# Optimization experiments

Measured on AMD Instinct MI355X. Metric: run time of the kernel, lower is better.

The kernel has to match this reference:

```python
import jax, jax.numpy as jnp
import numpy as np

HIDDEN = 2048
N_HEADS = 16
N_KV = 4
HEAD_DIM = 128
THETA = 500000.0
FREQ_ALLOC = 20  # t section; h = w = (HEAD_DIM//2 - 20)//2 = 22
T = 2048


def setup_inputs() -> dict:
    key = jax.random.key(0)
    k1, k2, k3, k4 = jax.random.split(key, 4)
    positions = jax.random.randint(k1, (3, T), 0, 1024, dtype=jnp.int32)
    hidden_states = jax.random.normal(k2, (T, HIDDEN), dtype=jnp.float32)
    w_qkv = jax.random.normal(k3, (HIDDEN, (N_HEADS + 2 * N_KV) * HEAD_DIM), dtype=jnp.float32) * 0.02
    w_o = jax.random.normal(k4, (N_HEADS * HEAD_DIM, HIDDEN), dtype=jnp.float32) * 0.02
    return {"positions": positions, "hidden_states": hidden_states, "w_qkv": w_qkv, "w_o": w_o}


def _mrope_cos_sin(positions):
    # standard rope table evaluated at positions: cos/sin each [3, T, HEAD_DIM//2]
    inv_freq = 1.0 / (THETA ** (jnp.arange(0, HEAD_DIM, 2, dtype=jnp.float32) / HEAD_DIM))
    freqs = positions.astype(jnp.float32)[..., None] * inv_freq
    cos, sin = jnp.cos(freqs), jnp.sin(freqs)
    sh = (HEAD_DIM // 2 - FREQ_ALLOC) // 2  # 22

    def section(c):
        c_t = c[0, :, -FREQ_ALLOC:]          # time dims from t-positions
        c_h = c[1, :, 0:2 * sh:2]            # even low-freq dims from h-positions
        c_w = c[2, :, 1:2 * sh:2]            # odd low-freq dims from w-positions
        c_hw = jnp.stack([c_h, c_w], axis=-1).reshape(c_h.shape[0], 2 * sh)
        return jnp.concatenate([c_hw, c_t], axis=-1)  # [T, HEAD_DIM//2]

    return section(cos), section(sin)


def _rotate_interleaved(x, cos, sin):
    # is_neox_style=False: even/odd interleaved rotation. x: [T, H, HEAD_DIM]
    x1, x2 = x[..., 0::2], x[..., 1::2]
    c, s = cos[:, None, :], sin[:, None, :]
    o1 = x1 * c - x2 * s
    o2 = x2 * c + x1 * s
    return jnp.stack([o1, o2], axis=-1).reshape(x.shape)


def reference(positions, hidden_states, w_qkv, w_o):
    q_size = N_HEADS * HEAD_DIM
    kv_size = N_KV * HEAD_DIM
    qkv = hidden_states @ w_qkv  # [T, 3072]
    q = qkv[:, :q_size].reshape(T, N_HEADS, HEAD_DIM)
    k = qkv[:, q_size:q_size + kv_size].reshape(T, N_KV, HEAD_DIM)
    v = qkv[:, q_size + kv_size:].reshape(T, N_KV, HEAD_DIM)

    cos, sin = _mrope_cos_sin(positions)
    q = _rotate_interleaved(q, cos, sin)
    k = _rotate_interleaved(k, cos, sin)

    # GQA causal attention
    rep = N_HEADS // N_KV
    kr = jnp.repeat(k, rep, axis=1)  # [T, N_HEADS, D]
    vr = jnp.repeat(v, rep, axis=1)
    scale = HEAD_DIM ** -0.5
    scores = jnp.einsum('qhd,khd->hqk', q, kr) * scale
    causal = jnp.tril(jnp.ones((T, T), dtype=bool))
    scores = jnp.where(causal[None], scores, jnp.finfo(scores.dtype).min)
    attn = jax.nn.softmax(scores, axis=-1)
    out = jnp.einsum('hqk,khd->qhd', attn, vr).reshape(T, N_HEADS * HEAD_DIM)
    return out @ w_o
```

## Files before the change

kernel.cpp:

```cpp
#include <hip/hip_runtime.h>
#include <math.h>

#define T 2048
#define HIDDEN 2048
#define NH 16
#define NKV 4
#define HD 128
#define QKV_N 3072
#define Q_SIZE 2048
#define KV_SIZE 512

typedef __attribute__((ext_vector_type(8))) short short8;
typedef __attribute__((ext_vector_type(4))) short short4v;
typedef __attribute__((ext_vector_type(4))) float floatx4;

__device__ __forceinline__ unsigned short f2bf(float f) {
    union { float f; unsigned int u; } v; v.f = f;
    unsigned int u = v.u;
    u += 0x7fffu + ((u >> 16) & 1u);
    return (unsigned short)(u >> 16);
}

__device__ __forceinline__ void gload_lds16(const unsigned short* g, unsigned short* l) {
    __builtin_amdgcn_global_load_lds((const __attribute__((address_space(1))) unsigned int*)g,
                                     (__attribute__((address_space(3))) unsigned int*)l, 16, 0, 0);
}

__global__ __launch_bounds__(256) void prep_misc(const float* __restrict__ hidden,
                                                 const float* __restrict__ w_qkv,
                                                 const float* __restrict__ w_o,
                                                 const int* __restrict__ positions,
                                                 unsigned short* __restrict__ hb,
                                                 unsigned short* __restrict__ wqt,
                                                 unsigned short* __restrict__ wot,
                                                 float* __restrict__ cosT,
                                                 float* __restrict__ sinT) {
    __shared__ float tile[32][33];
    const int b = blockIdx.x;
    const int tid = threadIdx.x;
    const int tx = tid & 31, ty = tid >> 5;

    if (b < 4096) {
        int i = (b * 256 + tid) * 4;
        float4 v = *(const float4*)(hidden + i);
        hb[i]     = f2bf(v.x);
        hb[i + 1] = f2bf(v.y);
        hb[i + 2] = f2bf(v.z);
        hb[i + 3] = f2bf(v.w);
    } else if (b < 10240) {
        int idx = b - 4096;
        int c0 = (idx % 96) * 32, r0 = (idx / 96) * 32;
#pragma unroll
        for (int i = 0; i < 4; ++i)
            tile[ty + i * 8][tx] = w_qkv[(long)(r0 + ty + i * 8) * QKV_N + c0 + tx];
        __syncthreads();
#pragma unroll
        for (int i = 0; i < 4; ++i)
            wqt[(long)(c0 + ty + i * 8) * HIDDEN + r0 + tx] = f2bf(tile[tx][ty + i * 8]);
    } else if (b < 14336) {
        int idx = b - 10240;
        int c0 = (idx % 64) * 32, r0 = (idx / 64) * 32;
#pragma unroll
        for (int i = 0; i < 4; ++i)
            tile[ty + i * 8][tx] = w_o[(long)(r0 + ty + i * 8) * HIDDEN + c0 + tx];
        __syncthreads();
#pragma unroll
        for (int i = 0; i < 4; ++i)
            wot[(long)(c0 + ty + i * 8) * HIDDEN + r0 + tx] = f2bf(tile[tx][ty + i * 8]);
    } else {
        int idx = b - 14336;
        int t = idx * 4 + (tid >> 6);
        int j = tid & 63;
        int row = (j >= 44) ? 0 : ((j & 1) ? 2 : 1);
        int pos = positions[row * T + t];
        float invf = exp2f((float)j * -0.29580571f);
        float ang = (float)pos * invf;
        cosT[t * 64 + j] = cosf(ang);
        sinT[t * 64 + j] = sinf(ang);
    }
}

__global__ __launch_bounds__(256) void gemm_qkv(const unsigned short* __restrict__ A,
                                                const unsigned short* __restrict__ B,
                                                const float* __restrict__ cosT,
                                                const float* __restrict__ sinT,
                                                unsigned short* __restrict__ qb,
                                                unsigned short* __restrict__ kb,
                                                unsigned short* __restrict__ vt) {
    __shared__ __align__(16) unsigned short As[2][64 * 32];
    __shared__ __align__(16) unsigned short Bs[2][128 * 32];
    const int K = HIDDEN;
    const int tid = threadIdx.x;
    const int wv = tid >> 6;
    const int lane = tid & 63;
    const int m = lane & 15, qd = lane >> 4;
    const unsigned short* Ab = A + (long)(blockIdx.x * 64) * K;
    const unsigned short* Bb = B + (long)(blockIdx.y * 128) * K;
    const int srow = tid >> 2;
    const int scol = (tid & 3) * 8;

    floatx4 acc[4][2];
#pragma unroll
    for (int i = 0; i < 4; ++i)
#pragma unroll
        for (int j = 0; j < 2; ++j) acc[i][j] = (floatx4){0.f, 0.f, 0.f, 0.f};

#define QKV_STAGE(buf, k0)                                                                \
    do {                                                                                  \
        gload_lds16(Ab + (long)srow * K + (k0) + scol,        &As[buf][wv * 512]);        \
        gload_lds16(Bb + (long)srow * K + (k0) + scol,        &Bs[buf][wv * 512]);        \
        gload_lds16(Bb + (long)(64 + srow) * K + (k0) + scol, &Bs[buf][2048 + wv * 512]); \
    } while (0)

    QKV_STAGE(0, 0);
    int cur = 0;
    for (int k0 = 0; k0 < K; k0 += 32) {
        __syncthreads();
        if (k0 + 32 < K) QKV_STAGE(cur ^ 1, k0 + 32);
        short8 a[4], b[2];
#pragma unroll
        for (int i = 0; i < 4; ++i) a[i] = *(const short8*)&As[cur][(i * 16 + m) * 32 + qd * 8];
#pragma unroll
        for (int j = 0; j < 2; ++j) b[j] = *(const short8*)&Bs[cur][(wv * 32 + j * 16 + m) * 32 + qd * 8];
#pragma unroll
        for (int i = 0; i < 4; ++i)
#pragma unroll
            for (int j = 0; j < 2; ++j)
                acc[i][j] = __builtin_amdgcn_mfma_f32_16x16x32_bf16(a[i], b[j], acc[i][j], 0, 0, 0);
        cur ^= 1;
    }
#undef QKV_STAGE

    const int by = blockIdx.y;
    if (by < 20) {
        const float sgn = (m & 1) ? 1.f : -1.f;
        const float qscale = 0.08838834764831845f;
#pragma unroll
        for (int i = 0; i < 4; ++i) {
#pragma unroll
            for (int r = 0; r < 4; ++r) {
                const int t = blockIdx.x * 64 + i * 16 + qd * 4 + r;
                const float* ct = cosT + t * 64;
                const float* st = sinT + t * 64;
#pragma unroll
                for (int j = 0; j < 2; ++j) {
                    const int cq = wv * 32 + j * 16 + m;
                    const int j2 = cq >> 1;
                    float val = acc[i][j][r];
                    float prt = __shfl_xor(val, 1);
                    float o = val * ct[j2] + sgn * prt * st[j2];
                    const int col = by * 128 + cq;
                    if (by < 16) qb[(long)t * Q_SIZE + col] = f2bf(o * qscale);
                    else         kb[(long)t * KV_SIZE + (col - 2048)] = f2bf(o);
                }
            }
        }
    } else {
        const int g = by - 20;
#pragma unroll
        for (int i = 0; i < 4; ++i)
#pragma unroll
            for (int j = 0; j < 2; ++j) {
                const int d = wv * 32 + j * 16 + m;
                const int t0 = blockIdx.x * 64 + i * 16 + qd * 4;
                unsigned short o4[4];
#pragma unroll
                for (int r = 0; r < 4; ++r) o4[r] = f2bf(acc[i][j][r]);
                *(short4v*)&vt[((long)g * HD + d) * T + t0] = *(short4v*)o4;
            }
    }
}

__global__ __launch_bounds__(256) void gemm_out(const unsigned short* __restrict__ A,
                                                const unsigned short* __restrict__ B,
                                                float* __restrict__ C,
                                                int K, int ldc) {
    __shared__ __align__(16) unsigned short As[2][64 * 32];
    __shared__ __align__(16) unsigned short Bs[2][128 * 32];
    const int tid = threadIdx.x;
    const int wv = tid >> 6;
    const int lane = tid & 63;
    const int m = lane & 15, qd = lane >> 4;
    const unsigned short* Ab = A + (long)(blockIdx.x * 64) * K;
    const unsigned short* Bb = B + (long)(blockIdx.y * 128) * K;
    const int srow = tid >> 2;
    const int scol = (tid & 3) * 8;

    floatx4 acc[4][2];
#pragma unroll
    for (int i = 0; i < 4; ++i)
#pragma unroll
        for (int j = 0; j < 2; ++j) acc[i][j] = (floatx4){0.f, 0.f, 0.f, 0.f};

#define OUT_STAGE(buf, k0)                                                                \
    do {                                                                                  \
        gload_lds16(Ab + (long)srow * K + (k0) + scol,        &As[buf][wv * 512]);        \
        gload_lds16(Bb + (long)srow * K + (k0) + scol,        &Bs[buf][wv * 512]);        \
        gload_lds16(Bb + (long)(64 + srow) * K + (k0) + scol, &Bs[buf][2048 + wv * 512]); \
    } while (0)

    OUT_STAGE(0, 0);
    int cur = 0;
    for (int k0 = 0; k0 < K; k0 += 32) {
        __syncthreads();
        if (k0 + 32 < K) OUT_STAGE(cur ^ 1, k0 + 32);
        short8 a[4], b[2];
#pragma unroll
        for (int i = 0; i < 4; ++i) a[i] = *(const short8*)&As[cur][(i * 16 + m) * 32 + qd * 8];
#pragma unroll
        for (int j = 0; j < 2; ++j) b[j] = *(const short8*)&Bs[cur][(wv * 32 + j * 16 + m) * 32 + qd * 8];
#pragma unroll
        for (int i = 0; i < 4; ++i)
#pragma unroll
            for (int j = 0; j < 2; ++j)
                acc[i][j] = __builtin_amdgcn_mfma_f32_16x16x32_bf16(a[i], b[j], acc[i][j], 0, 0, 0);
        cur ^= 1;
    }
#undef OUT_STAGE

#pragma unroll
    for (int i = 0; i < 4; ++i)
#pragma unroll
        for (int j = 0; j < 2; ++j)
#pragma unroll
            for (int r = 0; r < 4; ++r)
                C[(long)(blockIdx.x * 64 + i * 16 + qd * 4 + r) * ldc +
                  blockIdx.y * 128 + wv * 32 + j * 16 + m] = acc[i][j][r];
}

__global__ __launch_bounds__(256, 2) void flash_attn(const unsigned short* __restrict__ qb,
                                                     const unsigned short* __restrict__ kb,
                                                     const unsigned short* __restrict__ vt,
                                                     float* __restrict__ Opart,
                                                     float* __restrict__ MLpart) {
    __shared__ __align__(16) unsigned short Kbuf[2][64 * 128];
    __shared__ __align__(16) unsigned short Vbuf[128 * 64];
    __shared__ __align__(16) unsigned short Pls[4][32 * 72];

    const int tid = threadIdx.x;
    const int wv = tid >> 6;
    const int lane = tid & 63;
    const int m = lane & 15;
    const int qd = lane >> 4;

    const int h = blockIdx.x >> 4;
    const int c16 = blockIdx.x & 15;
    const int g = h >> 2;
    unsigned short* myP = Pls[wv];

    for (int seg = 0; seg < 2; ++seg) {
        const int qt = seg ? (15 - c16) : c16;
        const int half = seg;
        const int n0 = qt + 1;
        const int jt0 = half ? n0 : 0;
        const int jt1 = half ? 2 * qt + 2 : n0;
        const int q0 = qt * 128;

        short8 aq[2][4];
#pragma unroll
        for (int s = 0; s < 2; ++s)
#pragma unroll
            for (int kk = 0; kk < 4; ++kk)
                aq[s][kk] = *(const short8*)(qb + (long)(q0 + s * 64 + wv * 16 + m) * Q_SIZE +
                                             h * HD + kk * 32 + qd * 8);

        floatx4 acc_o[2][8];
#pragma unroll
        for (int s = 0; s < 2; ++s)
#pragma unroll
            for (int nb = 0; nb < 8; ++nb) acc_o[s][nb] = (floatx4){0.f, 0.f, 0.f, 0.f};
        float mrow[2] = {-1e30f, -1e30f};
        float lrow[2] = {0.f, 0.f};

#pragma unroll
        for (int i = 0; i < 4; ++i) {
            int s_ = i * 256 + tid;
            int r = s_ >> 4, c = (s_ & 15) ^ (r & 15);
            gload_lds16(kb + (long)(jt0 * 64 + r) * KV_SIZE + g * HD + c * 8,
                        &Kbuf[0][i * 2048 + wv * 512]);
        }
        int cur = 0;
        for (int jt = jt0; jt < jt1; ++jt) {
            __syncthreads();

            if (jt + 1 < jt1) {
#pragma unroll
                for (int i = 0; i < 4; ++i) {
                    int s_ = i * 256 + tid;
                    int r = s_ >> 4, c = (s_ & 15) ^ (r & 15);
                    gload_lds16(kb + (long)((jt + 1) * 64 + r) * KV_SIZE + g * HD + c * 8,
                                &Kbuf[cur ^ 1][i * 2048 + wv * 512]);
                }
            }
#pragma unroll
            for (int i = 0; i < 4; ++i) {
                int s_ = i * 256 + tid;
                int r = s_ >> 3, c = (s_ & 7) ^ (r & 7);
                gload_lds16(vt + ((long)g * HD + r) * T + jt * 64 + c * 8,
                            &Vbuf[i * 2048 + wv * 512]);
            }

            floatx4 acc_s[2][4];
#pragma unroll
            for (int s = 0; s < 2; ++s)
#pragma unroll
                for (int c = 0; c < 4; ++c) acc_s[s][c] = (floatx4){0.f, 0.f, 0.f, 0.f};
#pragma unroll
            for (int kk = 0; kk < 4; ++kk) {
#pragma unroll
                for (int c = 0; c < 4; ++c) {
                    short8 ak = *(const short8*)&Kbuf[cur][(c * 16 + m) * 128 +
                                                           (((4 * kk + qd) ^ m) * 8)];
                    acc_s[0][c] = __builtin_amdgcn_mfma_f32_16x16x32_bf16(ak, aq[0][kk], acc_s[0][c], 0, 0, 0);
                    acc_s[1][c] = __builtin_amdgcn_mfma_f32_16x16x32_bf16(ak, aq[1][kk], acc_s[1][c], 0, 0, 0);
                }
            }

#pragma unroll
            for (int s = 0; s < 2; ++s) {
                const int dg = 2 * qt + s;
                if (jt >= dg) {
                    const bool full = (jt > dg);
#pragma unroll
                    for (int c = 0; c < 4; ++c)
#pragma unroll
                        for (int r = 0; r < 4; ++r)
                            if (full || (c * 16 + qd * 4 + r > wv * 16 + m)) acc_s[s][c][r] = -1e30f;
                }
                float mx = acc_s[s][0][0];
#pragma unroll
                for (int c = 0; c < 4; ++c)
#pragma unroll
                    for (int r = 0; r < 4; ++r) mx = fmaxf(mx, acc_s[s][c][r]);
                mx = fmaxf(mx, __shfl_xor(mx, 16));
                mx = fmaxf(mx, __shfl_xor(mx, 32));
                float mnew = fmaxf(mrow[s], mx);
                float alpha = __expf(mrow[s] - mnew);
                mrow[s] = mnew;

                float pv[4][4];
                float lsum = 0.f;
#pragma unroll
                for (int c = 0; c < 4; ++c)
#pragma unroll
                    for (int r = 0; r < 4; ++r) {
                        pv[c][r] = __expf(acc_s[s][c][r] - mnew);
                        lsum += pv[c][r];
                    }
                lsum += __shfl_xor(lsum, 16);
                lsum += __shfl_xor(lsum, 32);
                lrow[s] = lrow[s] * alpha + lsum;
#pragma unroll
                for (int nb = 0; nb < 8; ++nb)
#pragma unroll
                    for (int r = 0; r < 4; ++r) acc_o[s][nb][r] *= alpha;
#pragma unroll
                for (int c = 0; c < 4; ++c) {
                    short4v pk = {(short)f2bf(pv[c][0]), (short)f2bf(pv[c][1]),
                                  (short)f2bf(pv[c][2]), (short)f2bf(pv[c][3])};
                    *(short4v*)&myP[(s * 16 + m) * 72 + c * 16 + qd * 4] = pk;
                }
            }

            __syncthreads();

#pragma unroll
            for (int kk = 0; kk < 2; ++kk) {
                short8 pa0 = *(const short8*)&myP[m * 72 + kk * 32 + qd * 8];
                short8 pa1 = *(const short8*)&myP[(16 + m) * 72 + kk * 32 + qd * 8];
#pragma unroll
                for (int nb = 0; nb < 8; ++nb) {
                    short8 av = *(const short8*)&Vbuf[(nb * 16 + m) * 64 +
                                                      (((4 * kk + qd) ^ (m & 7)) * 8)];
                    acc_o[0][nb] = __builtin_amdgcn_mfma_f32_16x16x32_bf16(av, pa0, acc_o[0][nb], 0, 0, 0);
                    acc_o[1][nb] = __builtin_amdgcn_mfma_f32_16x16x32_bf16(av, pa1, acc_o[1][nb], 0, 0, 0);
                }
            }
            cur ^= 1;
        }

        const int unit = (h * 16 + qt) * 2 + half;
#pragma unroll
        for (int s = 0; s < 2; ++s) {
            const long rb = (long)unit * 128 + s * 64 + wv * 16 + m;
#pragma unroll
            for (int nb = 0; nb < 8; ++nb)
                *(floatx4*)&Opart[rb * 128 + nb * 16 + qd * 4] = acc_o[s][nb];
            if (qd == 0) {
                MLpart[rb * 2]     = mrow[s];
                MLpart[rb * 2 + 1] = lrow[s];
            }
        }
    }
}

__global__ __launch_bounds__(256) void attn_combine(const float* __restrict__ Opart,
                                                    const float* __restrict__ MLpart,
                                                    unsigned short* __restrict__ ab) {
    const int tid = threadIdx.x;
    const int q = blockIdx.x * 16 + (tid >> 4);
    const int h = blockIdx.y;
    const int d0 = (tid & 15) * 8;
    const int qt = q >> 7, lr = q & 127;
    const long r0 = ((long)(h * 16 + qt) * 2) * 128 + lr;
    const long r1 = r0 + 128;
    float m0 = MLpart[r0 * 2], l0 = MLpart[r0 * 2 + 1];
    float m1 = MLpart[r1 * 2], l1 = MLpart[r1 * 2 + 1];
    float M = fmaxf(m0, m1);
    float a0 = __expf(m0 - M), a1 = __expf(m1 - M);
    float inv = 1.f / (l0 * a0 + l1 * a1);
    const float* O0 = Opart + r0 * 128 + d0;
    const float* O1 = Opart + r1 * 128 + d0;
    unsigned short outv[8];
#pragma unroll
    for (int j = 0; j < 8; j += 4) {
        float4 x0 = *(const float4*)(O0 + j);
        float4 x1 = *(const float4*)(O1 + j);
        outv[j]     = f2bf((x0.x * a0 + x1.x * a1) * inv);
        outv[j + 1] = f2bf((x0.y * a0 + x1.y * a1) * inv);
        outv[j + 2] = f2bf((x0.z * a0 + x1.z * a1) * inv);
        outv[j + 3] = f2bf((x0.w * a0 + x1.w * a1) * inv);
    }
    *(short8*)&ab[(long)q * Q_SIZE + h * HD + d0] = *(short8*)outv;
}

extern "C" void kernel_launch(void* const* d_in, const int* in_sizes, int n_in,
                              void* d_out, int out_size, void* d_ws, size_t ws_size,
                              hipStream_t stream) {
    const int* positions = (const int*)d_in[0];
    const float* hidden  = (const float*)d_in[1];
    const float* w_qkv   = (const float*)d_in[2];
    const float* w_o     = (const float*)d_in[3];
    float* out = (float*)d_out;

    char* p = (char*)d_ws;
    auto alloc = [&](size_t bytes) { char* r = p; p += (bytes + 255) & ~(size_t)255; return r; };
    float* cosT = (float*)alloc((size_t)T * 64 * 4);
    float* sinT = (float*)alloc((size_t)T * 64 * 4);
    unsigned short* hb  = (unsigned short*)alloc((size_t)T * HIDDEN * 2);
    unsigned short* wqt = (unsigned short*)alloc((size_t)QKV_N * HIDDEN * 2);
    unsigned short* wot = (unsigned short*)alloc((size_t)HIDDEN * HIDDEN * 2);
    unsigned short* qb  = (unsigned short*)alloc((size_t)T * Q_SIZE * 2);
    unsigned short* kb  = (unsigned short*)alloc((size_t)T * KV_SIZE * 2);
    unsigned short* vt  = (unsigned short*)alloc((size_t)T * KV_SIZE * 2);
    unsigned short* ab  = (unsigned short*)alloc((size_t)T * Q_SIZE * 2);
    float* Opart  = (float*)alloc((size_t)512 * 128 * 128 * 4);
    float* MLpart = (float*)alloc((size_t)512 * 128 * 2 * 4);

    prep_misc<<<dim3(14848), 256, 0, stream>>>(hidden, w_qkv, w_o, positions,
                                               hb, wqt, wot, cosT, sinT);
    gemm_qkv<<<dim3(T / 64, QKV_N / 128), 256, 0, stream>>>(hb, wqt, cosT, sinT, qb, kb, vt);
    flash_attn<<<dim3(256), 256, 0, stream>>>(qb, kb, vt, Opart, MLpart);
    attn_combine<<<dim3(T / 16, NH), 256, 0, stream>>>(Opart, MLpart, ab);
    gemm_out<<<dim3(T / 64, HIDDEN / 128), 256, 0, stream>>>(ab, wot, out, Q_SIZE, HIDDEN);
}
```

Before: 239.0 us.

## Drop split-KV partials and combine kernel; each block computes full q-tiles

```diff
diff --git a/kernel.cpp b/kernel.cpp
--- a/kernel.cpp
+++ b/kernel.cpp
@@ -231,8 +231,7 @@
 __global__ __launch_bounds__(256, 2) void flash_attn(const unsigned short* __restrict__ qb,
                                                      const unsigned short* __restrict__ kb,
                                                      const unsigned short* __restrict__ vt,
-                                                     float* __restrict__ Opart,
-                                                     float* __restrict__ MLpart) {
+                                                     unsigned short* __restrict__ ab) {
     __shared__ __align__(16) unsigned short Kbuf[2][64 * 128];
     __shared__ __align__(16) unsigned short Vbuf[128 * 64];
     __shared__ __align__(16) unsigned short Pls[4][32 * 72];
@@ -250,10 +249,7 @@
 
     for (int seg = 0; seg < 2; ++seg) {
         const int qt = seg ? (15 - c16) : c16;
-        const int half = seg;
-        const int n0 = qt + 1;
-        const int jt0 = half ? n0 : 0;
-        const int jt1 = half ? 2 * qt + 2 : n0;
+        const int jt1 = 2 * qt + 2;
         const int q0 = qt * 128;
 
         short8 aq[2][4];
@@ -276,11 +272,11 @@
         for (int i = 0; i < 4; ++i) {
             int s_ = i * 256 + tid;
             int r = s_ >> 4, c = (s_ & 15) ^ (r & 15);
-            gload_lds16(kb + (long)(jt0 * 64 + r) * KV_SIZE + g * HD + c * 8,
+            gload_lds16(kb + (long)r * KV_SIZE + g * HD + c * 8,
                         &Kbuf[0][i * 2048 + wv * 512]);
         }
         int cur = 0;
-        for (int jt = jt0; jt < jt1; ++jt) {
+        for (int jt = 0; jt < jt1; ++jt) {
             __syncthreads();
 
             if (jt + 1 < jt1) {
@@ -379,49 +375,19 @@
             cur ^= 1;
         }
 
-        const int unit = (h * 16 + qt) * 2 + half;
 #pragma unroll
         for (int s = 0; s < 2; ++s) {
-            const long rb = (long)unit * 128 + s * 64 + wv * 16 + m;
-#pragma unroll
-            for (int nb = 0; nb < 8; ++nb)
-                *(floatx4*)&Opart[rb * 128 + nb * 16 + qd * 4] = acc_o[s][nb];
-            if (qd == 0) {
-                MLpart[rb * 2]     = mrow[s];
-                MLpart[rb * 2 + 1] = lrow[s];
+            const float inv = 1.f / lrow[s];
+            const long trow = q0 + s * 64 + wv * 16 + m;
+#pragma unroll
+            for (int nb = 0; nb < 8; ++nb) {
+                unsigned short o4[4];
+#pragma unroll
+                for (int r = 0; r < 4; ++r) o4[r] = f2bf(acc_o[s][nb][r] * inv);
+                *(short4v*)&ab[trow * Q_SIZE + h * HD + nb * 16 + qd * 4] = *(short4v*)o4;
             }
         }
     }
-}
-
-__global__ __launch_bounds__(256) void attn_combine(const float* __restrict__ Opart,
-                                                    const float* __restrict__ MLpart,
-                                                    unsigned short* __restrict__ ab) {
-    const int tid = threadIdx.x;
-    const int q = blockIdx.x * 16 + (tid >> 4);
-    const int h = blockIdx.y;
-    const int d0 = (tid & 15) * 8;
-    const int qt = q >> 7, lr = q & 127;
-    const long r0 = ((long)(h * 16 + qt) * 2) * 128 + lr;
-    const long r1 = r0 + 128;
-    float m0 = MLpart[r0 * 2], l0 = MLpart[r0 * 2 + 1];
-    float m1 = MLpart[r1 * 2], l1 = MLpart[r1 * 2 + 1];
-    float M = fmaxf(m0, m1);
-    float a0 = __expf(m0 - M), a1 = __expf(m1 - M);
-    float inv = 1.f / (l0 * a0 + l1 * a1);
-    const float* O0 = Opart + r0 * 128 + d0;
-    const float* O1 = Opart + r1 * 128 + d0;
-    unsigned short outv[8];
-#pragma unroll
-    for (int j = 0; j < 8; j += 4) {
-        float4 x0 = *(const float4*)(O0 + j);
-        float4 x1 = *(const float4*)(O1 + j);
-        outv[j]     = f2bf((x0.x * a0 + x1.x * a1) * inv);
-        outv[j + 1] = f2bf((x0.y * a0 + x1.y * a1) * inv);
-        outv[j + 2] = f2bf((x0.z * a0 + x1.z * a1) * inv);
-        outv[j + 3] = f2bf((x0.w * a0 + x1.w * a1) * inv);
-    }
-    *(short8*)&ab[(long)q * Q_SIZE + h * HD + d0] = *(short8*)outv;
 }
 
 extern "C" void kernel_launch(void* const* d_in, const int* in_sizes, int n_in,
@@ -444,13 +410,10 @@
     unsigned short* kb  = (unsigned short*)alloc((size_t)T * KV_SIZE * 2);
     unsigned short* vt  = (unsigned short*)alloc((size_t)T * KV_SIZE * 2);
     unsigned short* ab  = (unsigned short*)alloc((size_t)T * Q_SIZE * 2);
-    float* Opart  = (float*)alloc((size_t)512 * 128 * 128 * 4);
-    float* MLpart = (float*)alloc((size_t)512 * 128 * 2 * 4);
 
     prep_misc<<<dim3(14848), 256, 0, stream>>>(hidden, w_qkv, w_o, positions,
                                                hb, wqt, wot, cosT, sinT);
     gemm_qkv<<<dim3(T / 64, QKV_N / 128), 256, 0, stream>>>(hb, wqt, cosT, sinT, qb, kb, vt);
-    flash_attn<<<dim3(256), 256, 0, stream>>>(qb, kb, vt, Opart, MLpart);
-    attn_combine<<<dim3(T / 16, NH), 256, 0, stream>>>(Opart, MLpart, ab);
+    flash_attn<<<dim3(256), 256, 0, stream>>>(qb, kb, vt, ab);
     gemm_out<<<dim3(T / 64, HIDDEN / 128), 256, 0, stream>>>(ab, wot, out, Q_SIZE, HIDDEN);
 }
```

New measurement: 265.5 us. +11.1%, slower.
